# Performance work log

Measured on AMD Instinct MI355X. Metric: run time of the kernel, lower is better.

## Reference

```python
import jax, jax.numpy as jnp
import numpy as np

D_MODEL = 1024
NUM_HEADS = 16
D_K = D_MODEL // NUM_HEADS
HEADS_DIST = [4, 4, 2, 2, 4]  # [token, statement, data_flow, control_flow, standard]
HYP_DF = 5.0
HYP_CF = 5.0
NEG_INF = -1000000000.0
B, S = 4, 1024


def _head_group_weights():
    # one-hot-per-group weight vectors of length NUM_HEADS
    ws = []
    start = 0
    for n in HEADS_DIST:
        w = np.zeros(NUM_HEADS, dtype=np.float32)
        w[start:start + n] = 1.0
        ws.append(jnp.asarray(w))
        start += n
    return ws  # tok_w, stmt_w, df_w, cf_w, std_w


def setup_inputs() -> dict:
    key = jax.random.key(0)
    ks = jax.random.split(key, 12)
    f32 = jnp.float32
    inp = {
        'Q': jax.random.normal(ks[0], (B, S, D_MODEL), f32),
        'K': jax.random.normal(ks[1], (B, S, D_MODEL), f32),
        'V': jax.random.normal(ks[2], (B, S, D_MODEL), f32),
        'token': jax.random.randint(ks[3], (B, S, S), 0, 2).astype(f32),
        'statement': jax.random.randint(ks[4], (B, S, S), 0, 2).astype(f32),
        'data_flow': jax.random.randint(ks[5], (B, S, S), 0, 2).astype(f32),
        'control_flow': jax.random.randint(ks[6], (B, S, S), 0, 2).astype(f32),
        'zero_matrix': jnp.zeros((B, S, S), f32),
        'mask': jax.random.randint(ks[7], (B, 1, S, S), 0, 2).astype(jnp.int32),
        # linear layer params (torch nn.Linear: y = x @ W.T + b)
        'Wq': jax.random.normal(ks[8], (D_MODEL, D_MODEL), f32) * 0.02,
        'bq': jnp.zeros((D_MODEL,), f32),
        'Wk': jax.random.normal(ks[9], (D_MODEL, D_MODEL), f32) * 0.02,
        'bk': jnp.zeros((D_MODEL,), f32),
        'Wv': jax.random.normal(ks[10], (D_MODEL, D_MODEL), f32) * 0.02,
        'bv': jnp.zeros((D_MODEL,), f32),
        'Wo': jax.random.normal(ks[11], (D_MODEL, D_MODEL), f32) * 0.02,
        'bo': jnp.zeros((D_MODEL,), f32),
    }
    return inp


def _split_heads(x):
    b, s, _ = x.shape
    return x.reshape(b, s, NUM_HEADS, D_K).transpose(0, 2, 1, 3)  # (B,H,S,dk)


def reference(Q, K, V, token, statement, data_flow, control_flow, zero_matrix,
              mask, Wq, bq, Wk, bk, Wv, bv, Wo, bo):
    tok_w, stmt_w, df_w, cf_w, _ = _head_group_weights()

    Qh = _split_heads(Q @ Wq.T + bq)
    Kh = _split_heads(K @ Wk.T + bk)
    Vh = _split_heads(V @ Wv.T + bv)

    scores = jnp.einsum('bhqd,bhkd->bhqk', Qh, Kh) / jnp.sqrt(jnp.float32(D_K))

    # local mask: -1e9 * token for token-heads, -1e9 * statement for statement-heads,
    # zero_matrix (zeros) elsewhere — expressed via per-head group weights instead of
    # the original redundant stack.
    w = lambda v: v[None, :, None, None]  # (1,H,1,1)
    local_mask = NEG_INF * (w(tok_w) * token[:, None] + w(stmt_w) * statement[:, None])
    # global enhance: |scores * (hyp_df*data_flow | hyp_cf*control_flow)| on their heads
    enhance_adj = (HYP_DF * w(df_w) * data_flow[:, None]
                   + HYP_CF * w(cf_w) * control_flow[:, None])
    global_enhance = jnp.abs(enhance_adj * scores)

    scores = scores + local_mask + global_enhance
    scores = jnp.where(mask == 0, NEG_INF, scores)

    probs = jax.nn.softmax(scores, axis=-1)  # (B,H,S,S)
    ctx = jnp.einsum('bhqk,bhkd->bhqd', probs, Vh)
    out = ctx.transpose(0, 2, 1, 3).reshape(B, S, D_MODEL)
    return out @ Wo.T + bo
```

## Files before the change

### kernel.cpp

```cpp
#include <hip/hip_runtime.h>
#include <stdint.h>

typedef unsigned short u16;
typedef unsigned int   u32;
typedef unsigned char  u8;
typedef __attribute__((ext_vector_type(4))) float f32x4;
typedef __attribute__((ext_vector_type(8))) __bf16 bf16x8;
typedef __attribute__((ext_vector_type(2))) unsigned int u32x2;
typedef __attribute__((ext_vector_type(4))) unsigned int u32x4;

#define MFMA16(a, b, c) __builtin_amdgcn_mfma_f32_16x16x32_bf16((a), (b), (c), 0, 0, 0)

__device__ __forceinline__ u16 f2bf(float f) {
  u32 u = __float_as_uint(f);
  return (u16)((u + 0x7fffu + ((u >> 16) & 1u)) >> 16);
}

__device__ __forceinline__ void gl_lds16(const void* g, void* l) {
  __builtin_amdgcn_global_load_lds((const __attribute__((address_space(1))) u32*)g,
                                   (__attribute__((address_space(3))) u32*)l, 16, 0, 0);
}

__device__ __forceinline__ u32 cvtpk(float a, float b) {
  u32 r;
  asm("v_cvt_pk_bf16_f32 %0, %1, %2" : "=v"(r) : "v"(a), "v"(b));
  return r;
}

__device__ __forceinline__ float exp2_hw(float x) {
  float r;
  asm("v_exp_f32 %0, %1" : "=v"(r) : "v"(x));
  return r;
}

__device__ __forceinline__ void plswap32(u32& x, u32& y) {
  u32x2 r = __builtin_amdgcn_permlane32_swap(x, y, false, false);
  x = r.x; y = r.y;
}
__device__ __forceinline__ void plswap16(u32& x, u32& y) {
  u32x2 r = __builtin_amdgcn_permlane16_swap(x, y, false, false);
  x = r.x; y = r.y;
}

__device__ __forceinline__ u32 pbit(float t, float s, float d, float c, int m) {
  const u32 nm = (m == 0) ? 1u : 0u;
  u32 r = (t != 0.0f ? 1u : 0u) | (s != 0.0f ? 2u : 0u) | (d != 0.0f ? 4u : 0u) |
          (c != 0.0f ? 8u : 0u) | ((1u - nm) << 4);
  r |= (((t != 0.0f ? 1u : 0u) | nm) << 5) | (((s != 0.0f ? 1u : 0u) | nm) << 6) | (nm << 7);
  return r;
}

__global__ void __launch_bounds__(256) pack_kernel(const float4* __restrict__ tok, const float4* __restrict__ st,
                                                   const float4* __restrict__ df, const float4* __restrict__ cf,
                                                   const int4* __restrict__ msk, u32* __restrict__ pko) {
  const int i = blockIdx.x * 256 + threadIdx.x;
  const int b = i >> 18, rem = i & 262143, q = rem >> 8, k4 = rem & 255;
  const int t = k4 >> 4, nk = (k4 >> 2) & 3, lg = k4 & 3;
  const u32 widx = ((u32)(b * 64 + (q >> 4)) * 16 + t) * 256 + (q & 15) * 16 + lg * 4 + nk;
  float4 vt = tok[i], vs = st[i], vd = df[i], vc = cf[i];
  int4 vm = msk[i];
  u32 b0 = pbit(vt.x, vs.x, vd.x, vc.x, vm.x);
  u32 b1 = pbit(vt.y, vs.y, vd.y, vc.y, vm.y);
  u32 b2 = pbit(vt.z, vs.z, vd.z, vc.z, vm.z);
  u32 b3 = pbit(vt.w, vs.w, vd.w, vc.w, vm.w);
  pko[widx] = b0 | (b1 << 8) | (b2 << 16) | (b3 << 24);
}

__global__ void __launch_bounds__(256) cvt_kernel(const float4* __restrict__ Q, const float4* __restrict__ K,
                                                  const float4* __restrict__ V, const float4* __restrict__ Wq,
                                                  const float4* __restrict__ Wk, const float4* __restrict__ Wv,
                                                  const float4* __restrict__ Wo, ushort4* __restrict__ oQ,
                                                  ushort4* __restrict__ oK, ushort4* __restrict__ oV,
                                                  ushort4* __restrict__ oWq, ushort4* __restrict__ oWk,
                                                  ushort4* __restrict__ oWv, ushort4* __restrict__ oWo) {
  const int bid = blockIdx.x;
  const float4* src;
  ushort4* dst;
  int base;
  if (bid < 1024)      { src = Q;  dst = oQ;  base = bid; }
  else if (bid < 2048) { src = K;  dst = oK;  base = bid - 1024; }
  else if (bid < 3072) { src = V;  dst = oV;  base = bid - 2048; }
  else if (bid < 3328) { src = Wq; dst = oWq; base = bid - 3072; }
  else if (bid < 3584) { src = Wk; dst = oWk; base = bid - 3328; }
  else if (bid < 3840) { src = Wv; dst = oWv; base = bid - 3584; }
  else                 { src = Wo; dst = oWo; base = bid - 3840; }
  const int i0 = base * 1024 + threadIdx.x;
#pragma unroll
  for (int u = 0; u < 4; u++) {
    const int i = i0 + u * 256;
    float4 v = src[i];
    dst[i] = make_ushort4(f2bf(v.x), f2bf(v.y), f2bf(v.z), f2bf(v.w));
  }
}

__global__ void __launch_bounds__(256) gemm_qkv(const u16* __restrict__ Abase, const u16* __restrict__ Wbase,
                                                const float* __restrict__ bq, const float* __restrict__ bk,
                                                const float* __restrict__ bv, u16* __restrict__ Obase) {
  __shared__ u16 smA[2][4096];
  __shared__ u16 smB[2][4096];
  const int fb = blockIdx.x;
  const int lid = (fb & 7) * 96 + (fb >> 3);
  const int z = lid >> 8;
  const int m0 = ((lid & 255) >> 3) * 128;
  const int n0 = (lid & 7) * 128;
  const u16* A = Abase + (size_t)z * 4194304;
  const u16* W = Wbase + (size_t)z * 1048576;
  const float* bias = (z == 0) ? bq : (z == 1) ? bk : bv;
  u16* Out = Obase + (size_t)z * 4194304;
  const int t = threadIdx.x;
  const int w = t >> 6, l = t & 63;
  const int l15 = l & 15, lg = l >> 4;
  const int wr = w >> 1, wc = w & 1;
  f32x4 acc[4][4] = {};
  const int srow = w * 16 + (l >> 2);
  const int scol_src = (((l & 3) ^ ((l >> 2) & 3))) * 8;
  const int scol_dst = (l & 3) * 8;
  const u16* Ab = A + (size_t)(m0 + srow) * 1024 + scol_src;
  const u16* Wb = W + (size_t)(n0 + srow) * 1024 + scol_src;
  const int soff = srow * 32 + scol_dst;
  const int c0g = (lg ^ (l15 & 3)) * 8;

  gl_lds16(Ab, &smA[0][soff]);
  gl_lds16(Ab + (size_t)64 * 1024, &smA[0][soff + 64 * 32]);
  gl_lds16(Wb, &smB[0][soff]);
  gl_lds16(Wb + (size_t)64 * 1024, &smB[0][soff + 64 * 32]);

  for (int it = 0; it < 32; it++) {
    __syncthreads();
    if (it < 31) {
      const int kk = (it + 1) * 32;
      const int nb = (it + 1) & 1;
      gl_lds16(Ab + kk, &smA[nb][soff]);
      gl_lds16(Ab + kk + (size_t)64 * 1024, &smA[nb][soff + 64 * 32]);
      gl_lds16(Wb + kk, &smB[nb][soff]);
      gl_lds16(Wb + kk + (size_t)64 * 1024, &smB[nb][soff + 64 * 32]);
    }
    const u16* bA = smA[it & 1];
    const u16* bB = smB[it & 1];
    bf16x8 af[4], bv_[4];
#pragma unroll
    for (int i = 0; i < 4; i++) af[i] = *(const bf16x8*)(bA + (wr * 64 + i * 16 + l15) * 32 + c0g);
#pragma unroll
    for (int i = 0; i < 4; i++) bv_[i] = *(const bf16x8*)(bB + (wc * 64 + i * 16 + l15) * 32 + c0g);
#pragma unroll
    for (int i = 0; i < 4; i++)
#pragma unroll
      for (int j = 0; j < 4; j++) acc[i][j] = MFMA16(af[i], bv_[j], acc[i][j]);
  }
#pragma unroll
  for (int j = 0; j < 4; j++) {
    const int n = n0 + wc * 64 + j * 16 + l15;
    const float bvj = bias[n];
#pragma unroll
    for (int i = 0; i < 4; i++) {
      const int mbase = m0 + wr * 64 + i * 16 + lg * 4;
      if (z < 2) {
#pragma unroll
        for (int r = 0; r < 4; r++) {
          const int m = mbase + r;
          Out[((size_t)((m >> 10) * 16 + (n >> 6)) << 16) + (size_t)(m & 1023) * 64 + (n & 63)] =
              f2bf(acc[i][j][r] + bvj);
        }
      } else {
        size_t off = ((size_t)((mbase >> 10) * 16 + (n >> 6)) << 16) + (size_t)(n & 63) * 1024 + (mbase & 1023);
        *(ushort4*)(Out + off) = make_ushort4(f2bf(acc[i][j][0] + bvj), f2bf(acc[i][j][1] + bvj),
                                              f2bf(acc[i][j][2] + bvj), f2bf(acc[i][j][3] + bvj));
      }
    }
  }
}

__global__ void __launch_bounds__(256) gemm_out(const u16* __restrict__ A, const u16* __restrict__ W,
                                                const float* __restrict__ bias, float* __restrict__ Out) {
  __shared__ u16 smA[2][4096];
  __shared__ u16 smB[2][4096];
  const int fb = blockIdx.x;
  const int lid = (fb & 7) * 32 + (fb >> 3);
  const int m0 = (lid >> 3) * 128;
  const int n0 = (lid & 7) * 128;
  const int t = threadIdx.x;
  const int w = t >> 6, l = t & 63;
  const int l15 = l & 15, lg = l >> 4;
  const int wr = w >> 1, wc = w & 1;
  f32x4 acc[4][4] = {};
  const int srow = w * 16 + (l >> 2);
  const int scol_src = (((l & 3) ^ ((l >> 2) & 3))) * 8;
  const int scol_dst = (l & 3) * 8;
  const u16* Ab = A + (size_t)(m0 + srow) * 1024 + scol_src;
  const u16* Wb = W + (size_t)(n0 + srow) * 1024 + scol_src;
  const int soff = srow * 32 + scol_dst;
  const int c0g = (lg ^ (l15 & 3)) * 8;

  gl_lds16(Ab, &smA[0][soff]);
  gl_lds16(Ab + (size_t)64 * 1024, &smA[0][soff + 64 * 32]);
  gl_lds16(Wb, &smB[0][soff]);
  gl_lds16(Wb + (size_t)64 * 1024, &smB[0][soff + 64 * 32]);

  for (int it = 0; it < 32; it++) {
    __syncthreads();
    if (it < 31) {
      const int kk = (it + 1) * 32;
      const int nb = (it + 1) & 1;
      gl_lds16(Ab + kk, &smA[nb][soff]);
      gl_lds16(Ab + kk + (size_t)64 * 1024, &smA[nb][soff + 64 * 32]);
      gl_lds16(Wb + kk, &smB[nb][soff]);
      gl_lds16(Wb + kk + (size_t)64 * 1024, &smB[nb][soff + 64 * 32]);
    }
    const u16* bA = smA[it & 1];
    const u16* bB = smB[it & 1];
    bf16x8 af[4], bv_[4];
#pragma unroll
    for (int i = 0; i < 4; i++) af[i] = *(const bf16x8*)(bA + (wr * 64 + i * 16 + l15) * 32 + c0g);
#pragma unroll
    for (int i = 0; i < 4; i++) bv_[i] = *(const bf16x8*)(bB + (wc * 64 + i * 16 + l15) * 32 + c0g);
#pragma unroll
    for (int i = 0; i < 4; i++)
#pragma unroll
      for (int j = 0; j < 4; j++) acc[i][j] = MFMA16(af[i], bv_[j], acc[i][j]);
  }
#pragma unroll
  for (int j = 0; j < 4; j++) {
    const int n = n0 + wc * 64 + j * 16 + l15;
    const float bvj = bias[n];
#pragma unroll
    for (int i = 0; i < 4; i++) {
      const int mbase = m0 + wr * 64 + i * 16 + lg * 4;
#pragma unroll
      for (int r = 0; r < 4; r++) Out[(size_t)(mbase + r) * 1024 + n] = acc[i][j][r] + bvj;
    }
  }
}

__global__ void __launch_bounds__(256) attn_kernel(const u16* __restrict__ Qp, const u16* __restrict__ Kp,
                                                   const u16* __restrict__ Vt, const u8* __restrict__ pack,
                                                   u16* __restrict__ ctx) {
  __shared__ u16 smK[2][4096];
  __shared__ u16 smV[2][4096];
  const float SCL  = 0.18033688011112042f;
  const float FMX  = 32.0f;
  const int tid = threadIdx.x;
  const int w = tid >> 6, l = tid & 63;
  const int l15 = l & 15, lg = l >> 4;
  const int f = blockIdx.x;
  const int swz = (f & 7) * 128 + (f >> 3);
  const int bh = swz >> 4, bx = swz & 15;
  const int b = bh >> 4, h = bh & 15;
  const int q0 = bx * 64 + w * 16;
  const bool enh = (h >= 8 && h < 12);
  const u32 kbit = (h < 4) ? 0x20u : (h < 8) ? 0x40u : 0x80u;
  const u32 ebit = (h < 10) ? 0x04u : 0x08u;
  const u32 kb_[4] = {kbit, kbit << 8, kbit << 16, kbit << 24};
  const u32 eb_[4] = {ebit, ebit << 8, ebit << 16, ebit << 24};
  const size_t hb = (size_t)bh << 16;
  const u32x4 onesw = {0x3F803F80u, 0x3F803F80u, 0x3F803F80u, 0x3F803F80u};
  const bf16x8 ones_frag = __builtin_bit_cast(bf16x8, onesw);

  bf16x8 qf[2];
#pragma unroll
  for (int ks = 0; ks < 2; ks++)
    qf[ks] = *(const bf16x8*)(Qp + hb + (size_t)(q0 + l15) * 64 + ks * 32 + lg * 8);

  const int srow = w * 16 + (l >> 3);
  const int schunk = (l & 7) ^ (l >> 3);
  const u16* Ksrc = Kp + hb + (size_t)srow * 64 + schunk * 8;
  const u16* Vsrc = Vt + hb + (size_t)srow * 1024 + schunk * 8;
  const int c0 = (lg ^ (l15 & 7)) * 8;
  const u8* pkq = pack + ((size_t)((b * 64 + bx * 4 + w) * 16)) * 1024 + (l15 * 4 + lg) * 16;

  gl_lds16(Ksrc, &smK[0][w * 1024]);
  gl_lds16(Ksrc + 512, &smK[0][w * 1024 + 512]);
  gl_lds16(Vsrc, &smV[0][w * 1024]);
  gl_lds16(Vsrc + 8192, &smV[0][w * 1024 + 512]);
  uint4 pk_next = *(const uint4*)(pkq);

  f32x4 octx[4] = {};
  f32x4 osum = {};

  for (int t = 0; t < 16; t++) {
    __syncthreads();
    const uint4 pkc = pk_next;
    if (t < 15) {
      const int kb = (t + 1) * 64;
      const int nb = (t + 1) & 1;
      gl_lds16(Ksrc + (size_t)kb * 64, &smK[nb][w * 1024]);
      gl_lds16(Ksrc + (size_t)kb * 64 + 512, &smK[nb][w * 1024 + 512]);
      gl_lds16(Vsrc + kb, &smV[nb][w * 1024]);
      gl_lds16(Vsrc + kb + 8192, &smV[nb][w * 1024 + 512]);
      pk_next = *(const uint4*)(pkq + (t + 1) * 1024);
    }
    const u16* bK = smK[t & 1];
    const u16* bV = smV[t & 1];
    f32x4 sc[4];
    __builtin_amdgcn_s_setprio(1);
#pragma unroll
    for (int nk = 0; nk < 4; nk++) {
      const u16* kr = bK + (nk * 16 + l15) * 64;
      bf16x8 kf0 = *(const bf16x8*)(kr + c0);
      bf16x8 kf1 = *(const bf16x8*)(kr + (c0 ^ 32));
      f32x4 z = {0.0f, 0.0f, 0.0f, 0.0f};
      z = MFMA16(kf0, qf[0], z);
      z = MFMA16(kf1, qf[1], z);
      sc[nk] = z;
    }
    __builtin_amdgcn_s_setprio(0);
    const u32 pkw[4] = {pkc.x, pkc.y, pkc.z, pkc.w};
#pragma unroll
    for (int nk = 0; nk < 4; nk++)
#pragma unroll
      for (int r = 0; r < 4; r++) {
        float s;
        if (enh) {
          float tt = sc[nk][r] * SCL;
          tt = (pkw[nk] & eb_[r]) ? __builtin_fmaf(fabsf(tt), 5.0f, tt) : tt;
          s = tt - FMX;
        } else {
          s = __builtin_fmaf(sc[nk][r], SCL, -FMX);
        }
        float p = exp2_hw(s);
        p = (pkw[nk] & kb_[r]) ? 0.0f : p;
        sc[nk][r] = p;
      }
    __builtin_amdgcn_s_setprio(1);
#pragma unroll
    for (int kk = 0; kk < 2; kk++) {
      u32 a0 = cvtpk(sc[2 * kk][0], sc[2 * kk][1]);
      u32 a1 = cvtpk(sc[2 * kk][2], sc[2 * kk][3]);
      u32 b0 = cvtpk(sc[2 * kk + 1][0], sc[2 * kk + 1][1]);
      u32 b1 = cvtpk(sc[2 * kk + 1][2], sc[2 * kk + 1][3]);
      plswap32(a0, b0);
      plswap32(a1, b1);
      plswap16(a0, b0);
      plswap16(a1, b1);
      u32x4 wv = {a0, a1, b0, b1};
      bf16x8 pfrag = __builtin_bit_cast(bf16x8, wv);
      osum = MFMA16(ones_frag, pfrag, osum);
#pragma unroll
      for (int nd = 0; nd < 4; nd++) {
        bf16x8 vf = *(const bf16x8*)(bV + (nd * 16 + l15) * 64 + (c0 ^ (kk * 32)));
        octx[nd] = MFMA16(vf, pfrag, octx[nd]);
      }
    }
    __builtin_amdgcn_s_setprio(0);
  }
  const float inv = 1.0f / fmaxf(osum[0], 1e-35f);
  u16* cb = ctx + (size_t)b * 1048576 + (size_t)(q0 + l15) * 1024 + h * 64 + lg * 4;
#pragma unroll
  for (int nd = 0; nd < 4; nd++) {
    *(ushort4*)(cb + nd * 16) = make_ushort4(f2bf(octx[nd][0] * inv), f2bf(octx[nd][1] * inv),
                                             f2bf(octx[nd][2] * inv), f2bf(octx[nd][3] * inv));
  }
}

extern "C" void kernel_launch(void* const* d_in, const int* in_sizes, int n_in,
                              void* d_out, int out_size, void* d_ws, size_t ws_size,
                              hipStream_t stream) {
  (void)in_sizes; (void)n_in; (void)out_size; (void)ws_size;
  const float* Q  = (const float*)d_in[0];
  const float* K  = (const float*)d_in[1];
  const float* V  = (const float*)d_in[2];
  const float* tok = (const float*)d_in[3];
  const float* st  = (const float*)d_in[4];
  const float* df  = (const float*)d_in[5];
  const float* cf  = (const float*)d_in[6];
  const int*   msk = (const int*)d_in[8];
  const float* Wq = (const float*)d_in[9];
  const float* bq = (const float*)d_in[10];
  const float* Wk = (const float*)d_in[11];
  const float* bk = (const float*)d_in[12];
  const float* Wv = (const float*)d_in[13];
  const float* bv = (const float*)d_in[14];
  const float* Wo = (const float*)d_in[15];
  const float* bo = (const float*)d_in[16];

  char* ws = (char*)d_ws;
  const size_t MB = 1ull << 20;
  u16* Qbf = (u16*)(ws);
  u16* Wqb = (u16*)(ws + 24 * MB);
  u8*  pkQ = (u8*)(ws + 32 * MB);
  u16* Qh  = (u16*)(ws + 36 * MB);
  u16* ctx = (u16*)(ws + 60 * MB);
  u16* Kbf = Qbf + 4194304;
  u16* Vbf = Qbf + 8388608;
  u16* Wkb = Wqb + 1048576;
  u16* Wvb = Wqb + 2097152;
  u16* Wob = Wqb + 3145728;

  pack_kernel<<<4096, 256, 0, stream>>>((const float4*)tok, (const float4*)st, (const float4*)df,
                                        (const float4*)cf, (const int4*)msk, (u32*)pkQ);
  cvt_kernel<<<4096, 256, 0, stream>>>((const float4*)Q, (const float4*)K, (const float4*)V,
                                       (const float4*)Wq, (const float4*)Wk, (const float4*)Wv, (const float4*)Wo,
                                       (ushort4*)Qbf, (ushort4*)Kbf, (ushort4*)Vbf,
                                       (ushort4*)Wqb, (ushort4*)Wkb, (ushort4*)Wvb, (ushort4*)Wob);
  gemm_qkv<<<768, 256, 0, stream>>>(Qbf, Wqb, bq, bk, bv, Qh);
  attn_kernel<<<1024, 256, 0, stream>>>(Qh, Qh + 4194304, Qh + 8388608, pkQ, ctx);
  gemm_out<<<256, 256, 0, stream>>>(ctx, Wob, bo, (float*)d_out);
}
```

Before: 132.7 us.

## Triple-buffer LDS tiles in QKV and output GEMMs with explicit vmcnt waits

Both projection GEMMs move from double to triple buffering of their A/W tiles in LDS, so tiles are prefetched two K-steps ahead. The generic __syncthreads is replaced by an explicit `s_waitcnt vmcnt(4)` plus `s_barrier`, fenced by sched_barrier, so each wave waits only for the tile it is about to read while the next tile's loads stay in flight. The aim is to hide global-load latency behind the MFMA work. In exchange, LDS per block grows from 32 KB to 48 KB, which may lower occupancy. The last two iterations also issue redundant wrapped-around loads into buffers that are never read.

```diff
diff --git a/kernel.cpp b/kernel.cpp
--- a/kernel.cpp
+++ b/kernel.cpp
@@ -10,6 +10,7 @@
 typedef __attribute__((ext_vector_type(4))) unsigned int u32x4;
 
 #define MFMA16(a, b, c) __builtin_amdgcn_mfma_f32_16x16x32_bf16((a), (b), (c), 0, 0, 0)
+#define SCHED0() __builtin_amdgcn_sched_barrier(0)
 
 __device__ __forceinline__ u16 f2bf(float f) {
   u32 u = __float_as_uint(f);
@@ -96,8 +97,8 @@
 __global__ void __launch_bounds__(256) gemm_qkv(const u16* __restrict__ Abase, const u16* __restrict__ Wbase,
                                                 const float* __restrict__ bq, const float* __restrict__ bk,
                                                 const float* __restrict__ bv, u16* __restrict__ Obase) {
-  __shared__ u16 smA[2][4096];
-  __shared__ u16 smB[2][4096];
+  __shared__ u16 smA[3][4096];
+  __shared__ u16 smB[3][4096];
   const int fb = blockIdx.x;
   const int lid = (fb & 7) * 96 + (fb >> 3);
   const int z = lid >> 8;
@@ -120,23 +121,28 @@
   const int soff = srow * 32 + scol_dst;
   const int c0g = (lg ^ (l15 & 3)) * 8;
 
-  gl_lds16(Ab, &smA[0][soff]);
-  gl_lds16(Ab + (size_t)64 * 1024, &smA[0][soff + 64 * 32]);
-  gl_lds16(Wb, &smB[0][soff]);
-  gl_lds16(Wb + (size_t)64 * 1024, &smB[0][soff + 64 * 32]);
-
+#define QKV_STAGE(ti, bf)                                          \
+  do {                                                             \
+    const int kk_ = (ti) * 32;                                     \
+    gl_lds16(Ab + kk_, &smA[bf][soff]);                            \
+    gl_lds16(Ab + kk_ + (size_t)64 * 1024, &smA[bf][soff + 2048]); \
+    gl_lds16(Wb + kk_, &smB[bf][soff]);                            \
+    gl_lds16(Wb + kk_ + (size_t)64 * 1024, &smB[bf][soff + 2048]); \
+  } while (0)
+
+  QKV_STAGE(0, 0);
+  QKV_STAGE(1, 1);
+
+  int b2 = 2;
   for (int it = 0; it < 32; it++) {
-    __syncthreads();
-    if (it < 31) {
-      const int kk = (it + 1) * 32;
-      const int nb = (it + 1) & 1;
-      gl_lds16(Ab + kk, &smA[nb][soff]);
-      gl_lds16(Ab + kk + (size_t)64 * 1024, &smA[nb][soff + 64 * 32]);
-      gl_lds16(Wb + kk, &smB[nb][soff]);
-      gl_lds16(Wb + kk + (size_t)64 * 1024, &smB[nb][soff + 64 * 32]);
-    }
-    const u16* bA = smA[it & 1];
-    const u16* bB = smB[it & 1];
+    SCHED0();
+    asm volatile("s_waitcnt vmcnt(4)" ::: "memory");
+    __builtin_amdgcn_s_barrier();
+    SCHED0();
+    QKV_STAGE((it + 2) & 31, b2);
+    const u16* bA = smA[b2 == 2 ? 0 : b2 + 1];
+    const u16* bB = smB[b2 == 2 ? 0 : b2 + 1];
+    b2 = (b2 == 2) ? 0 : b2 + 1;
     bf16x8 af[4], bv_[4];
 #pragma unroll
     for (int i = 0; i < 4; i++) af[i] = *(const bf16x8*)(bA + (wr * 64 + i * 16 + l15) * 32 + c0g);
@@ -147,6 +153,7 @@
 #pragma unroll
       for (int j = 0; j < 4; j++) acc[i][j] = MFMA16(af[i], bv_[j], acc[i][j]);
   }
+#undef QKV_STAGE
 #pragma unroll
   for (int j = 0; j < 4; j++) {
     const int n = n0 + wc * 64 + j * 16 + l15;
@@ -172,8 +179,8 @@
 
 __global__ void __launch_bounds__(256) gemm_out(const u16* __restrict__ A, const u16* __restrict__ W,
                                                 const float* __restrict__ bias, float* __restrict__ Out) {
-  __shared__ u16 smA[2][4096];
-  __shared__ u16 smB[2][4096];
+  __shared__ u16 smA[3][4096];
+  __shared__ u16 smB[3][4096];
   const int fb = blockIdx.x;
   const int lid = (fb & 7) * 32 + (fb >> 3);
   const int m0 = (lid >> 3) * 128;
@@ -191,23 +198,28 @@
   const int soff = srow * 32 + scol_dst;
   const int c0g = (lg ^ (l15 & 3)) * 8;
 
-  gl_lds16(Ab, &smA[0][soff]);
-  gl_lds16(Ab + (size_t)64 * 1024, &smA[0][soff + 64 * 32]);
-  gl_lds16(Wb, &smB[0][soff]);
-  gl_lds16(Wb + (size_t)64 * 1024, &smB[0][soff + 64 * 32]);
-
+#define OUT_STAGE(ti, bf)                                          \
+  do {                                                             \
+    const int kk_ = (ti) * 32;                                     \
+    gl_lds16(Ab + kk_, &smA[bf][soff]);                            \
+    gl_lds16(Ab + kk_ + (size_t)64 * 1024, &smA[bf][soff + 2048]); \
+    gl_lds16(Wb + kk_, &smB[bf][soff]);                            \
+    gl_lds16(Wb + kk_ + (size_t)64 * 1024, &smB[bf][soff + 2048]); \
+  } while (0)
+
+  OUT_STAGE(0, 0);
+  OUT_STAGE(1, 1);
+
+  int b2 = 2;
   for (int it = 0; it < 32; it++) {
-    __syncthreads();
-    if (it < 31) {
-      const int kk = (it + 1) * 32;
-      const int nb = (it + 1) & 1;
-      gl_lds16(Ab + kk, &smA[nb][soff]);
-      gl_lds16(Ab + kk + (size_t)64 * 1024, &smA[nb][soff + 64 * 32]);
-      gl_lds16(Wb + kk, &smB[nb][soff]);
-      gl_lds16(Wb + kk + (size_t)64 * 1024, &smB[nb][soff + 64 * 32]);
-    }
-    const u16* bA = smA[it & 1];
-    const u16* bB = smB[it & 1];
+    SCHED0();
+    asm volatile("s_waitcnt vmcnt(4)" ::: "memory");
+    __builtin_amdgcn_s_barrier();
+    SCHED0();
+    OUT_STAGE((it + 2) & 31, b2);
+    const u16* bA = smA[b2 == 2 ? 0 : b2 + 1];
+    const u16* bB = smB[b2 == 2 ? 0 : b2 + 1];
+    b2 = (b2 == 2) ? 0 : b2 + 1;
     bf16x8 af[4], bv_[4];
 #pragma unroll
     for (int i = 0; i < 4; i++) af[i] = *(const bf16x8*)(bA + (wr * 64 + i * 16 + l15) * 32 + c0g);
@@ -218,6 +230,7 @@
 #pragma unroll
       for (int j = 0; j < 4; j++) acc[i][j] = MFMA16(af[i], bv_[j], acc[i][j]);
   }
+#undef OUT_STAGE
 #pragma unroll
   for (int j = 0; j < 4; j++) {
     const int n = n0 + wc * 64 + j * 16 + l15;
```

Result: slower. 142.2 us (+7.2%).
